# Kernel tuning notes

Hardware: AMD Instinct MI355X
Metric: run time of the kernel (lower is better)

The kernel has to match this reference:

```python
import jax, jax.numpy as jnp
import numpy as np

# CycleFC1w1a constants (from init_kwargs / gen_offset)
IN_CH = 384
KH, KW = 1, 7  # cycle kernel; actual conv weight is 1x1
START = (KH * KW) // 2  # 3


def _gen_offset_x(C):
    # kernel_size[0] == 1 branch: off_y = 0, off_x[i] = (i + START) % KW - KW // 2
    i = jnp.arange(C)
    return (i + START) % KW - KW // 2  # int32, values in [-3, 3]


def setup_inputs() -> dict:
    key = jax.random.key(0)
    k1, k2, k3 = jax.random.split(key, 3)
    x = jax.random.normal(k1, (64, IN_CH, 32, 32), dtype=jnp.float32)
    weight = jax.random.normal(k2, (IN_CH, IN_CH), dtype=jnp.float32) * 0.05  # [out_ch, in_ch]
    bias = jax.random.normal(k3, (IN_CH,), dtype=jnp.float32) * 0.01
    return {"x": x, "weight": weight, "bias": bias}


def reference(x, weight, bias):
    B, C, H, W = x.shape
    # BinaryQuantizer forward: sign()
    xb = jnp.sign(x)
    wb = jnp.sign(weight)  # [O, C]

    # Fixed per-channel integer horizontal offsets -> exact shifted gather
    off_x = _gen_offset_x(C)                                  # [C]
    cols = jnp.arange(W)[None, :] + off_x[:, None]            # [C, W] sample col = w + off
    valid = (cols >= 0) & (cols < W)                          # zero-pad out of bounds
    cols_c = jnp.clip(cols, 0, W - 1)
    # gather along width per channel: [B, C, H, W]
    g = jnp.take_along_axis(xb, cols_c[None, :, None, :], axis=3)
    g = g * valid[None, :, None, :].astype(x.dtype)

    # pointwise (1x1) channel-mixing conv
    out = jnp.einsum('bchw,oc->bohw', g, wb) + bias[None, :, None, None]
    return out
```

## Files before the change

### kernel.cpp

```cpp
#include <hip/hip_runtime.h>
#include <stdint.h>


#define IN_CH 384
#define HH 32
#define WW 32
#define BB 64

constexpr uint64_t P7(int t) {
  uint64_t m = 0;
  for (int k = 0; k < 64; ++k)
    if (k % 7 == t) m |= (1ull << k);
  return m;
}
__device__ __constant__ uint64_t Pm[7] = {P7(0), P7(1), P7(2), P7(3), P7(4), P7(5), P7(6)};

__global__ __launch_bounds__(64) void cyc_prep(const float* __restrict__ wgt,
                                               const float* __restrict__ bias,
                                               uint64_t* __restrict__ wbg,
                                               float* __restrict__ bias2t) {
  const int o = blockIdx.x;
  const int lane = threadIdx.x;
  __shared__ uint64_t wb_sh[6];
#pragma unroll
  for (int j = 0; j < 6; ++j) {
    uint64_t m = __ballot(wgt[o * IN_CH + j * 64 + lane] < 0.0f);
    if (lane == 0) wb_sh[j] = m;
  }
  __syncthreads();
  if (lane < 6) wbg[o * 6 + lane] = wb_sh[lane];
  if (lane < WW) {
    const int w = lane;
    int nv = 0, corr = 0;
#pragma unroll
    for (int j = 0; j < 6; ++j) {
      uint64_t V = 0;
#pragma unroll
      for (int d = -3; d <= 3; ++d) {
        int wd = w + d;
        if (wd >= 0 && wd < WW) V |= Pm[(d - j + 14) % 7];
      }
      nv += __popcll(V);
      corr += __popcll(wb_sh[j] & ~V);
    }
    bias2t[w * IN_CH + o] = bias[o] + (float)nv + 2.0f * (float)corr;
  }
}

__global__ __launch_bounds__(384, 4) void cyc_fused(const float* __restrict__ x,
                                                    const uint64_t* __restrict__ wbg,
                                                    const float* __restrict__ bias2t,
                                                    float* __restrict__ out) {
  __shared__ uint32_t sh_G[12][2][WW];
  const int t = threadIdx.x;
  const int b = blockIdx.x >> 4;
  const int h0 = (blockIdx.x & 15) * 2;
  const int wave = t >> 6, lane = t & 63;

  {
    const int j = wave;
    const int c = j * 64 + lane;
    const int cm = c % 7;
    const int off = ((cm + 3) % 7) - 3;
    const uint32_t shr = (off > 0) ? (uint32_t)off : 0u;
    const uint32_t shl = (off < 0) ? (uint32_t)(-off) : 0u;
#pragma unroll
    for (int r = 0; r < 2; ++r) {
      const float4* xp = reinterpret_cast<const float4*>(
          x + (size_t)((b * IN_CH + c) * HH + h0 + r) * WW);
      uint32_t myw = 0;
#pragma unroll
      for (int i = 0; i < 8; ++i) {
        float4 v = xp[i];
        myw |= (v.x < 0.0f ? 1u : 0u) << (i * 4 + 0);
        myw |= (v.y < 0.0f ? 1u : 0u) << (i * 4 + 1);
        myw |= (v.z < 0.0f ? 1u : 0u) << (i * 4 + 2);
        myw |= (v.w < 0.0f ? 1u : 0u) << (i * 4 + 3);
      }
      uint32_t s = (myw >> shr) << shl;
      constexpr uint32_t Mt[5] = {0xFFFF0000u, 0xFF00FF00u, 0xF0F0F0F0u,
                                  0xCCCCCCCCu, 0xAAAAAAAAu};
#pragma unroll
      for (int stp = 0; stp < 5; ++stp) {
        const int js = 16 >> stp;
        const uint32_t M = Mt[stp];
        uint32_t y = __shfl_xor(s, js);
        s = (lane & js) ? ((s & M) | ((y >> js) & ~M))
                        : ((s & ~M) | ((y << js) & M));
      }
      sh_G[2 * j + (lane >> 5)][r][lane & 31] = s;
    }
  }
  __syncthreads();

  const int og = __builtin_amdgcn_readfirstlane(wave);
  const int w = lane & 31, r2 = lane >> 5;
  uint64_t g[6];
#pragma unroll
  for (int jj = 0; jj < 6; ++jj) {
    uint32_t lo = sh_G[2 * jj + 0][r2][w];
    uint32_t hi = sh_G[2 * jj + 1][r2][w];
    g[jj] = ((uint64_t)hi << 32) | (uint64_t)lo;
  }
#pragma unroll
  for (int half = 0; half < 2; ++half) {
    const int ob = og * 64 + half * 32;
    float bb[32];
    {
      const float4* bsrc =
          reinterpret_cast<const float4*>(bias2t + w * IN_CH + ob);
      float4* bdst = reinterpret_cast<float4*>(bb);
#pragma unroll
      for (int i = 0; i < 8; ++i) bdst[i] = bsrc[i];
    }
    const uint64_t* wp = wbg + (size_t)ob * 6;
    float* op = out + ((size_t)b * IN_CH + ob) * (HH * WW) + h0 * WW + lane;
#pragma unroll
    for (int i = 0; i < 32; ++i) {
      const uint64_t w0 = wp[i * 6 + 0], w1 = wp[i * 6 + 1], w2 = wp[i * 6 + 2];
      const uint64_t w3 = wp[i * 6 + 3], w4 = wp[i * 6 + 4], w5 = wp[i * 6 + 5];
      int mm = __popcll(g[0] ^ w0) + __popcll(g[1] ^ w1) + __popcll(g[2] ^ w2) +
               __popcll(g[3] ^ w3) + __popcll(g[4] ^ w4) + __popcll(g[5] ^ w5);
      op[i * (HH * WW)] = bb[i] - 2.0f * (float)mm;
    }
  }
}

extern "C" void kernel_launch(void* const* d_in, const int* in_sizes, int n_in,
                              void* d_out, int out_size, void* d_ws, size_t ws_size,
                              hipStream_t stream) {
  const float* x = (const float*)d_in[0];
  const float* wgt = (const float*)d_in[1];
  const float* bias = (const float*)d_in[2];
  float* out = (float*)d_out;

  uint64_t* wbg = (uint64_t*)d_ws;
  float* bias2t = (float*)((char*)d_ws + 18432);

  cyc_prep<<<IN_CH, 64, 0, stream>>>(wgt, bias, wbg, bias2t);
  cyc_fused<<<BB * (HH / 2), 384, 0, stream>>>(x, wbg, bias2t, out);
}
```

Baseline: 206.0 us.

## Retile fused binary conv to 8 rows per block and split outputs in halves

Each block now packs 8 image rows of sign bits into shared memory, stored in a per-pixel layout with all channel words adjacent. Each wave computes 32 output channels for 4 row positions, so every weight word it loads is reused across 4 XOR-popcount accumulations. The output channels are split across two blocks per (batch, row group), which means the sign packing of x is done twice and x is read twice. Occupancy hint drops from 4 to 3 because the extra g registers raise register pressure.

```diff
diff --git a/kernel.cpp b/kernel.cpp
--- a/kernel.cpp
+++ b/kernel.cpp
@@ -6,6 +6,7 @@
 #define HH 32
 #define WW 32
 #define BB 64
+#define HRB 8
 
 constexpr uint64_t P7(int t) {
   uint64_t m = 0;
@@ -47,25 +48,29 @@
   }
 }
 
-__global__ __launch_bounds__(384, 4) void cyc_fused(const float* __restrict__ x,
+__global__ __launch_bounds__(384, 3) void cyc_fused(const float* __restrict__ x,
                                                     const uint64_t* __restrict__ wbg,
                                                     const float* __restrict__ bias2t,
                                                     float* __restrict__ out) {
-  __shared__ uint32_t sh_G[12][2][WW];
+  __shared__ uint64_t sh_G[HRB][WW][6];
   const int t = threadIdx.x;
-  const int b = blockIdx.x >> 4;
-  const int h0 = (blockIdx.x & 15) * 2;
+  const int bid = blockIdx.x;
+  const int oh = bid & 1;
+  const int hgrp = (bid >> 1) & 3;
+  const int b = bid >> 3;
+  const int h0 = hgrp * HRB;
   const int wave = t >> 6, lane = t & 63;
 
   {
     const int j = wave;
     const int c = j * 64 + lane;
-    const int cm = c % 7;
-    const int off = ((cm + 3) % 7) - 3;
+    const int off = ((c % 7 + 3) % 7) - 3;
     const uint32_t shr = (off > 0) ? (uint32_t)off : 0u;
     const uint32_t shl = (off < 0) ? (uint32_t)(-off) : 0u;
+    uint32_t* shw = (uint32_t*)sh_G;
+    const int h = lane >> 5, wcol = lane & 31;
 #pragma unroll
-    for (int r = 0; r < 2; ++r) {
+    for (int r = 0; r < HRB; ++r) {
       const float4* xp = reinterpret_cast<const float4*>(
           x + (size_t)((b * IN_CH + c) * HH + h0 + r) * WW);
       uint32_t myw = 0;
@@ -88,41 +93,48 @@
         s = (lane & js) ? ((s & M) | ((y >> js) & ~M))
                         : ((s & ~M) | ((y << js) & M));
       }
-      sh_G[2 * j + (lane >> 5)][r][lane & 31] = s;
+      shw[((r * WW + wcol) * 6 + j) * 2 + h] = s;
     }
   }
   __syncthreads();
 
   const int og = __builtin_amdgcn_readfirstlane(wave);
   const int w = lane & 31, r2 = lane >> 5;
-  uint64_t g[6];
+  uint64_t g[4][6];
 #pragma unroll
-  for (int jj = 0; jj < 6; ++jj) {
-    uint32_t lo = sh_G[2 * jj + 0][r2][w];
-    uint32_t hi = sh_G[2 * jj + 1][r2][w];
-    g[jj] = ((uint64_t)hi << 32) | (uint64_t)lo;
+  for (int p = 0; p < 4; ++p) {
+    const ulonglong2* gv =
+        reinterpret_cast<const ulonglong2*>(&sh_G[p * 2 + r2][w][0]);
+    ulonglong2 a0 = gv[0], a1 = gv[1], a2 = gv[2];
+    g[p][0] = a0.x; g[p][1] = a0.y; g[p][2] = a1.x;
+    g[p][3] = a1.y; g[p][4] = a2.x; g[p][5] = a2.y;
   }
+  const int ob = oh * 192 + og * 32;
+  float bb[32];
+  {
+    const float4* bsrc = reinterpret_cast<const float4*>(bias2t + w * IN_CH + ob);
+    float4* bdst = reinterpret_cast<float4*>(bb);
 #pragma unroll
-  for (int half = 0; half < 2; ++half) {
-    const int ob = og * 64 + half * 32;
-    float bb[32];
-    {
-      const float4* bsrc =
-          reinterpret_cast<const float4*>(bias2t + w * IN_CH + ob);
-      float4* bdst = reinterpret_cast<float4*>(bb);
+    for (int i = 0; i < 8; ++i) bdst[i] = bsrc[i];
+  }
+  const uint64_t* wp = wbg + (size_t)ob * 6;
+  float* op = out + ((size_t)b * IN_CH + ob) * (HH * WW) + h0 * WW + lane;
 #pragma unroll
-      for (int i = 0; i < 8; ++i) bdst[i] = bsrc[i];
-    }
-    const uint64_t* wp = wbg + (size_t)ob * 6;
-    float* op = out + ((size_t)b * IN_CH + ob) * (HH * WW) + h0 * WW + lane;
-#pragma unroll
-    for (int i = 0; i < 32; ++i) {
-      const uint64_t w0 = wp[i * 6 + 0], w1 = wp[i * 6 + 1], w2 = wp[i * 6 + 2];
-      const uint64_t w3 = wp[i * 6 + 3], w4 = wp[i * 6 + 4], w5 = wp[i * 6 + 5];
-      int mm = __popcll(g[0] ^ w0) + __popcll(g[1] ^ w1) + __popcll(g[2] ^ w2) +
-               __popcll(g[3] ^ w3) + __popcll(g[4] ^ w4) + __popcll(g[5] ^ w5);
-      op[i * (HH * WW)] = bb[i] - 2.0f * (float)mm;
-    }
+  for (int i = 0; i < 32; ++i) {
+    const uint64_t w0 = wp[i * 6 + 0], w1 = wp[i * 6 + 1], w2 = wp[i * 6 + 2];
+    const uint64_t w3 = wp[i * 6 + 3], w4 = wp[i * 6 + 4], w5 = wp[i * 6 + 5];
+    int m0 = __popcll(g[0][0] ^ w0) + __popcll(g[0][1] ^ w1) + __popcll(g[0][2] ^ w2) +
+             __popcll(g[0][3] ^ w3) + __popcll(g[0][4] ^ w4) + __popcll(g[0][5] ^ w5);
+    int m1 = __popcll(g[1][0] ^ w0) + __popcll(g[1][1] ^ w1) + __popcll(g[1][2] ^ w2) +
+             __popcll(g[1][3] ^ w3) + __popcll(g[1][4] ^ w4) + __popcll(g[1][5] ^ w5);
+    int m2 = __popcll(g[2][0] ^ w0) + __popcll(g[2][1] ^ w1) + __popcll(g[2][2] ^ w2) +
+             __popcll(g[2][3] ^ w3) + __popcll(g[2][4] ^ w4) + __popcll(g[2][5] ^ w5);
+    int m3 = __popcll(g[3][0] ^ w0) + __popcll(g[3][1] ^ w1) + __popcll(g[3][2] ^ w2) +
+             __popcll(g[3][3] ^ w3) + __popcll(g[3][4] ^ w4) + __popcll(g[3][5] ^ w5);
+    op[i * (HH * WW) + 0]   = bb[i] - 2.0f * (float)m0;
+    op[i * (HH * WW) + 64]  = bb[i] - 2.0f * (float)m1;
+    op[i * (HH * WW) + 128] = bb[i] - 2.0f * (float)m2;
+    op[i * (HH * WW) + 192] = bb[i] - 2.0f * (float)m3;
   }
 }
 
@@ -138,5 +150,5 @@
   float* bias2t = (float*)((char*)d_ws + 18432);
 
   cyc_prep<<<IN_CH, 64, 0, stream>>>(wgt, bias, wbg, bias2t);
-  cyc_fused<<<BB * (HH / 2), 384, 0, stream>>>(x, wbg, bias2t, out);
+  cyc_fused<<<BB * (HH / HRB) * 2, 384, 0, stream>>>(x, wbg, bias2t, out);
 }
```

New measurement: 208.6 us. About the same (+1.3%).

## Process four rows per block with 12 waves and reuse weights across row pairs

Applied to the files above, without the earlier changes.

Each block now covers four image rows with 768 threads (12 waves), so each wave handles 32 output channels for two row pairs. Every weight bitmask load is reused for two popcount dot products. The packed sign bits go into shared memory as contiguous 64-bit words, read back with vector LDS loads. This halves the weight and bias reload traffic per output but raises registers per thread and lowers the block count, which may hurt occupancy.

```diff
diff --git a/kernel.cpp b/kernel.cpp
--- a/kernel.cpp
+++ b/kernel.cpp
@@ -6,6 +6,7 @@
 #define HH 32
 #define WW 32
 #define BB 64
+#define HR 4
 
 constexpr uint64_t P7(int t) {
   uint64_t m = 0;
@@ -47,25 +48,27 @@
   }
 }
 
-__global__ __launch_bounds__(384, 4) void cyc_fused(const float* __restrict__ x,
-                                                    const uint64_t* __restrict__ wbg,
-                                                    const float* __restrict__ bias2t,
-                                                    float* __restrict__ out) {
-  __shared__ uint32_t sh_G[12][2][WW];
+__global__ __launch_bounds__(768) void cyc_fused(const float* __restrict__ x,
+                                                 const uint64_t* __restrict__ wbg,
+                                                 const float* __restrict__ bias2t,
+                                                 float* __restrict__ out) {
+  __shared__ uint64_t sh_G[HR][WW][6];
   const int t = threadIdx.x;
-  const int b = blockIdx.x >> 4;
-  const int h0 = (blockIdx.x & 15) * 2;
+  const int b = blockIdx.x >> 3;
+  const int h0 = (blockIdx.x & 7) * HR;
   const int wave = t >> 6, lane = t & 63;
 
   {
-    const int j = wave;
-    const int c = j * 64 + lane;
-    const int cm = c % 7;
-    const int off = ((cm + 3) % 7) - 3;
-    const uint32_t shr = (off > 0) ? (uint32_t)off : 0u;
-    const uint32_t shl = (off < 0) ? (uint32_t)(-off) : 0u;
+    uint32_t* shw = (uint32_t*)sh_G;
+    const int h = lane >> 5, wcol = lane & 31;
 #pragma unroll
-    for (int r = 0; r < 2; ++r) {
+    for (int p = 0; p < 2; ++p) {
+      const int tau = wave + p * 12;
+      const int r = tau / 6, j = tau % 6;
+      const int c = j * 64 + lane;
+      const int off = ((c % 7 + 3) % 7) - 3;
+      const uint32_t shr = (off > 0) ? (uint32_t)off : 0u;
+      const uint32_t shl = (off < 0) ? (uint32_t)(-off) : 0u;
       const float4* xp = reinterpret_cast<const float4*>(
           x + (size_t)((b * IN_CH + c) * HH + h0 + r) * WW);
       uint32_t myw = 0;
@@ -88,40 +91,42 @@
         s = (lane & js) ? ((s & M) | ((y >> js) & ~M))
                         : ((s & ~M) | ((y << js) & M));
       }
-      sh_G[2 * j + (lane >> 5)][r][lane & 31] = s;
+      shw[((r * WW + wcol) * 6 + j) * 2 + h] = s;
     }
   }
   __syncthreads();
 
   const int og = __builtin_amdgcn_readfirstlane(wave);
   const int w = lane & 31, r2 = lane >> 5;
-  uint64_t g[6];
+  const ulonglong2* gv = reinterpret_cast<const ulonglong2*>(&sh_G[r2][w][0]);
+  const ulonglong2 a0 = gv[0], a1 = gv[1], a2 = gv[2];
+  const ulonglong2* hv = reinterpret_cast<const ulonglong2*>(&sh_G[2 + r2][w][0]);
+  const ulonglong2 b0 = hv[0], b1 = hv[1], b2 = hv[2];
+  const uint64_t gA0 = a0.x, gA1 = a0.y, gA2 = a1.x, gA3 = a1.y, gA4 = a2.x, gA5 = a2.y;
+  const uint64_t gB0 = b0.x, gB1 = b0.y, gB2 = b1.x, gB3 = b1.y, gB4 = b2.x, gB5 = b2.y;
+
+  const float4* bsrc = reinterpret_cast<const float4*>(bias2t + w * IN_CH + og * 32);
+  const uint64_t* wp = wbg + (size_t)og * 32 * 6;
+  float* opA = out + ((size_t)b * IN_CH + og * 32) * (HH * WW) + h0 * WW + lane;
+  float* opB = opA + 2 * WW;
+
 #pragma unroll
-  for (int jj = 0; jj < 6; ++jj) {
-    uint32_t lo = sh_G[2 * jj + 0][r2][w];
-    uint32_t hi = sh_G[2 * jj + 1][r2][w];
-    g[jj] = ((uint64_t)hi << 32) | (uint64_t)lo;
-  }
+  for (int ot = 0; ot < 4; ++ot) {
+    const float4 bb0 = bsrc[ot * 2 + 0];
+    const float4 bb1 = bsrc[ot * 2 + 1];
+    const float bbv[8] = {bb0.x, bb0.y, bb0.z, bb0.w,
+                          bb1.x, bb1.y, bb1.z, bb1.w};
 #pragma unroll
-  for (int half = 0; half < 2; ++half) {
-    const int ob = og * 64 + half * 32;
-    float bb[32];
-    {
-      const float4* bsrc =
-          reinterpret_cast<const float4*>(bias2t + w * IN_CH + ob);
-      float4* bdst = reinterpret_cast<float4*>(bb);
-#pragma unroll
-      for (int i = 0; i < 8; ++i) bdst[i] = bsrc[i];
-    }
-    const uint64_t* wp = wbg + (size_t)ob * 6;
-    float* op = out + ((size_t)b * IN_CH + ob) * (HH * WW) + h0 * WW + lane;
-#pragma unroll
-    for (int i = 0; i < 32; ++i) {
-      const uint64_t w0 = wp[i * 6 + 0], w1 = wp[i * 6 + 1], w2 = wp[i * 6 + 2];
-      const uint64_t w3 = wp[i * 6 + 3], w4 = wp[i * 6 + 4], w5 = wp[i * 6 + 5];
-      int mm = __popcll(g[0] ^ w0) + __popcll(g[1] ^ w1) + __popcll(g[2] ^ w2) +
-               __popcll(g[3] ^ w3) + __popcll(g[4] ^ w4) + __popcll(g[5] ^ w5);
-      op[i * (HH * WW)] = bb[i] - 2.0f * (float)mm;
+    for (int i = 0; i < 8; ++i) {
+      const int oi = ot * 8 + i;
+      const uint64_t w0 = wp[oi * 6 + 0], w1 = wp[oi * 6 + 1], w2 = wp[oi * 6 + 2];
+      const uint64_t w3 = wp[oi * 6 + 3], w4 = wp[oi * 6 + 4], w5 = wp[oi * 6 + 5];
+      int mmA = __popcll(gA0 ^ w0) + __popcll(gA1 ^ w1) + __popcll(gA2 ^ w2) +
+                __popcll(gA3 ^ w3) + __popcll(gA4 ^ w4) + __popcll(gA5 ^ w5);
+      int mmB = __popcll(gB0 ^ w0) + __popcll(gB1 ^ w1) + __popcll(gB2 ^ w2) +
+                __popcll(gB3 ^ w3) + __popcll(gB4 ^ w4) + __popcll(gB5 ^ w5);
+      opA[oi * (HH * WW)] = bbv[i] - 2.0f * (float)mmA;
+      opB[oi * (HH * WW)] = bbv[i] - 2.0f * (float)mmB;
     }
   }
 }
@@ -138,5 +143,5 @@
   float* bias2t = (float*)((char*)d_ws + 18432);
 
   cyc_prep<<<IN_CH, 64, 0, stream>>>(wgt, bias, wbg, bias2t);
-  cyc_fused<<<BB * (HH / 2), 384, 0, stream>>>(x, wbg, bias2t, out);
+  cyc_fused<<<BB * (HH / HR), 768, 0, stream>>>(x, wbg, bias2t, out);
 }
```

Result: faster. 196.9 us (-4.4%).
